# Kernel tuning notes

Measured on AMD Instinct MI355X. Metric: run time of the kernel, lower is better.

The kernel has to match this reference:

```python
import jax, jax.numpy as jnp
import numpy as np

B, T, C, H = 4, 2048, 1024, 16
HS = C // H  # head size 64
LN_EPS = 1e-5


def setup_inputs() -> dict:
    key = jax.random.key(0)
    ks = jax.random.split(key, 14)
    s = lambda fan_in: 1.0 / np.sqrt(fan_in)
    return {
        "x": jax.random.normal(ks[0], (B, T, C), jnp.float32),
        # weights stored [in, out] (transposed vs torch nn.Linear) for y = x @ W + b
        "c_attn_w": jax.random.normal(ks[1], (C, 3 * C), jnp.float32) * s(C),
        "c_attn_b": jnp.zeros((3 * C,), jnp.float32),
        "c_proj_w": jax.random.normal(ks[2], (C, C), jnp.float32) * s(C),
        "c_proj_b": jnp.zeros((C,), jnp.float32),
        "fc_w": jax.random.normal(ks[3], (C, 4 * C), jnp.float32) * s(C),
        "fc_b": jnp.zeros((4 * C,), jnp.float32),
        "proj_w": jax.random.normal(ks[4], (4 * C, C), jnp.float32) * s(4 * C),
        "proj_b": jnp.zeros((C,), jnp.float32),
        "ln1_g": jnp.ones((C,), jnp.float32),
        "ln1_b": jnp.zeros((C,), jnp.float32),
        "ln2_g": jnp.ones((C,), jnp.float32),
        "ln2_b": jnp.zeros((C,), jnp.float32),
    }


def layer_norm(x, g, b):
    mu = jnp.mean(x, axis=-1, keepdims=True)
    var = jnp.var(x, axis=-1, keepdims=True)
    return (x - mu) * jax.lax.rsqrt(var + LN_EPS) * g + b


def attention(x, c_attn_w, c_attn_b, c_proj_w, c_proj_b):
    Bs, Ts, Cs = x.shape
    qkv = x @ c_attn_w + c_attn_b  # (B,T,3C)
    q, k, v = jnp.split(qkv, 3, axis=-1)
    q = q.reshape(Bs, Ts, H, HS).transpose(0, 2, 1, 3)  # (B,H,T,hs)
    k = k.reshape(Bs, Ts, H, HS).transpose(0, 2, 1, 3)
    v = v.reshape(Bs, Ts, H, HS).transpose(0, 2, 1, 3)
    wei = jnp.einsum("bhqd,bhkd->bhqk", q, k) * (1.0 / np.sqrt(HS))
    causal = jnp.tril(jnp.ones((Ts, Ts), bool))
    wei = jnp.where(causal, wei, -jnp.inf)
    wei = jax.nn.softmax(wei, axis=-1)
    out = jnp.einsum("bhqk,bhkd->bhqd", wei, v)
    out = out.transpose(0, 2, 1, 3).reshape(Bs, Ts, Cs)
    return out @ c_proj_w + c_proj_b


def mlp(x, fc_w, fc_b, proj_w, proj_b):
    h = jax.nn.gelu(x @ fc_w + fc_b, approximate=True)
    return h @ proj_w + proj_b


def reference(x, c_attn_w, c_attn_b, c_proj_w, c_proj_b, fc_w, fc_b, proj_w, proj_b, ln1_g, ln1_b, ln2_g, ln2_b):
    x = x + attention(layer_norm(x, ln1_g, ln1_b), c_attn_w, c_attn_b, c_proj_w, c_proj_b)
    out = x + mlp(layer_norm(x, ln2_g, ln2_b), fc_w, fc_b, proj_w, proj_b)
    return out
```

## Files before the change

### kernel.cpp

```cpp
#include <hip/hip_runtime.h>

typedef unsigned short u16;
typedef __attribute__((ext_vector_type(8))) short bf16x8;
typedef __attribute__((ext_vector_type(4))) float f32x4;

#define SC_LOG2E 0.18033688011112043f
#define MB_LOG2E 17.31234049066756f

__device__ __forceinline__ float b2f(u16 u) {
  union { unsigned int i; float f; } v; v.i = ((unsigned int)u) << 16; return v.f;
}
__device__ __forceinline__ u16 f2b(float f) {
  unsigned int x = __float_as_uint(f);
  unsigned int r = (x + 0x7fffu + ((x >> 16) & 1u)) >> 16;
  return (u16)r;
}

#define GLOAD_LDS16(g, l)                                                              \
  __builtin_amdgcn_global_load_lds((const __attribute__((address_space(1))) void*)(g), \
                                   (__attribute__((address_space(3))) void*)(l), 16, 0, 0)

__global__ __launch_bounds__(256) void transpose_cast_kernel(const float* __restrict__ in,
                                                             u16* __restrict__ out,
                                                             int K, int N) {
  __shared__ float tile[64][65];
  const int tid = threadIdx.x;
  const int n0 = blockIdx.x * 64, k0 = blockIdx.y * 64;
#pragma unroll
  for (int it = 0; it < 4; ++it) {
    int lin = it * 256 + tid;
    int r = lin >> 4, c4 = (lin & 15) * 4;
    float4 v = *(const float4*)&in[(size_t)(k0 + r) * N + n0 + c4];
    tile[r][c4 + 0] = v.x; tile[r][c4 + 1] = v.y;
    tile[r][c4 + 2] = v.z; tile[r][c4 + 3] = v.w;
  }
  __syncthreads();
#pragma unroll
  for (int it = 0; it < 2; ++it) {
    int lin = it * 256 + tid;
    int r = lin >> 3, c8 = (lin & 7) * 8;
    u16 tmp[8];
#pragma unroll
    for (int j = 0; j < 8; ++j) tmp[j] = f2b(tile[c8 + j][r]);
    *(uint4*)&out[(size_t)(n0 + r) * K + k0 + c8] = *(const uint4*)tmp;
  }
}

__global__ __launch_bounds__(256) void transpose_v_kernel(const u16* __restrict__ qkv,
                                                          u16* __restrict__ vt) {
  __shared__ float tl[64][65];
  const int tid = threadIdx.x;
  const int bh = blockIdx.y, b = bh >> 4, h = bh & 15;
  const int t0 = blockIdx.x * 64;
  const int voff = 2048 + h * 64;
#pragma unroll
  for (int it = 0; it < 2; ++it) {
    int lin = it * 256 + tid;
    int tt = lin >> 3, d8 = (lin & 7) * 8;
    uint4 v = *(const uint4*)&qkv[((size_t)b * 2048 + t0 + tt) * 3072 + voff + d8];
    const u16* p = (const u16*)&v;
#pragma unroll
    for (int j = 0; j < 8; ++j) tl[tt][d8 + j] = b2f(p[j]);
  }
  __syncthreads();
#pragma unroll
  for (int it = 0; it < 2; ++it) {
    int lin = it * 256 + tid;
    int d = lin >> 3, t8 = (lin & 7) * 8;
    u16 tmp[8];
#pragma unroll
    for (int j = 0; j < 8; ++j) tmp[j] = f2b(tl[t8 + j][d]);
    *(uint4*)&vt[((size_t)bh * 64 + d) * 2048 + t0 + t8] = *(const uint4*)tmp;
  }
}

template <bool INF32>
__global__ __launch_bounds__(256) void ln_kernel(const void* __restrict__ xv,
                                                 const float* __restrict__ g,
                                                 const float* __restrict__ b,
                                                 u16* __restrict__ o, int C) {
  const int row = blockIdx.x, tid = threadIdx.x;
  const int wave = tid >> 6, lane = tid & 63;
  const int base = tid * 4;
  float f[4];
  if (INF32) {
    float4 v = *(const float4*)((const float*)xv + (size_t)row * C + base);
    f[0] = v.x; f[1] = v.y; f[2] = v.z; f[3] = v.w;
  } else {
    ushort4 v = *(const ushort4*)((const u16*)xv + (size_t)row * C + base);
    f[0] = b2f(v.x); f[1] = b2f(v.y); f[2] = b2f(v.z); f[3] = b2f(v.w);
  }
  float s = f[0] + f[1] + f[2] + f[3];
  float q = f[0] * f[0] + f[1] * f[1] + f[2] * f[2] + f[3] * f[3];
#pragma unroll
  for (int off = 1; off < 64; off <<= 1) {
    s += __shfl_xor(s, off);
    q += __shfl_xor(q, off);
  }
  __shared__ float reds[4], redq[4];
  if (lane == 0) { reds[wave] = s; redq[wave] = q; }
  __syncthreads();
  float S = reds[0] + reds[1] + reds[2] + reds[3];
  float Q = redq[0] + redq[1] + redq[2] + redq[3];
  const float inv = 1.0f / (float)C;
  float mean = S * inv;
  float var = Q * inv - mean * mean;
  float rs = rsqrtf(var + 1e-5f);
  float4 gv = *(const float4*)&g[base];
  float4 bv = *(const float4*)&b[base];
  ushort4 ov;
  ov.x = f2b((f[0] - mean) * rs * gv.x + bv.x);
  ov.y = f2b((f[1] - mean) * rs * gv.y + bv.y);
  ov.z = f2b((f[2] - mean) * rs * gv.z + bv.z);
  ov.w = f2b((f[3] - mean) * rs * gv.w + bv.w);
  *(ushort4*)&o[(size_t)row * C + base] = ov;
}

__device__ __forceinline__ float gelu_fn(float v) {
  float a = 0.7978845608028654f * __builtin_fmaf(0.044715f * v * v, v, v);
  float t = __builtin_amdgcn_exp2f(a * -2.8853900817779268f);
  return v * __builtin_amdgcn_rcpf(1.0f + t);
}

template <bool GELU, int RESMODE, bool OUTF32>
__global__ __launch_bounds__(256) void gemm_kernel(const u16* __restrict__ A,
                                                   const u16* __restrict__ Bt,
                                                   const float* __restrict__ bias,
                                                   const void* __restrict__ res,
                                                   void* __restrict__ Cv,
                                                   int M, int N, int K) {
  __shared__ u16 As[128 * 64];
  __shared__ u16 Bs[128 * 64];
  const int tid = threadIdx.x;
  const int wave = tid >> 6, lane = tid & 63;
  const int lhi = lane >> 4, llo = lane & 15;
  const int sw = llo & 7;
  const int m0 = blockIdx.x * 128, n0 = blockIdx.y * 128;
  const int wr = (wave >> 1) * 64, wc = (wave & 1) * 64;

  f32x4 acc[4][4] = {};

  for (int k0 = 0; k0 < K; k0 += 64) {
#pragma unroll
    for (int p = 0; p < 4; ++p) {
      int s = p * 256 + tid;
      int r = s >> 3;
      int c = ((s & 7) ^ (r & 7)) * 8;
      GLOAD_LDS16(A + (size_t)(m0 + r) * K + k0 + c, As + s * 8);
      GLOAD_LDS16(Bt + (size_t)(n0 + r) * K + k0 + c, Bs + s * 8);
    }
    __syncthreads();
#pragma unroll
    for (int kk = 0; kk < 2; ++kk) {
      const int cp = ((kk * 4 + lhi) ^ sw) * 8;
      bf16x8 af[4], bf[4];
#pragma unroll
      for (int i = 0; i < 4; ++i)
        af[i] = *(const bf16x8*)&As[(wr + i * 16 + llo) * 64 + cp];
#pragma unroll
      for (int j = 0; j < 4; ++j)
        bf[j] = *(const bf16x8*)&Bs[(wc + j * 16 + llo) * 64 + cp];
#pragma unroll
      for (int i = 0; i < 4; ++i)
#pragma unroll
        for (int j = 0; j < 4; ++j)
          acc[i][j] = __builtin_amdgcn_mfma_f32_16x16x32_bf16(af[i], bf[j], acc[i][j], 0, 0, 0);
    }
    __syncthreads();
  }

#pragma unroll
  for (int i = 0; i < 4; ++i) {
    int row = m0 + wr + i * 16 + lhi * 4;
#pragma unroll
    for (int j = 0; j < 4; ++j) {
      int col = n0 + wc + j * 16 + llo;
      float bv = bias[col];
#pragma unroll
      for (int r = 0; r < 4; ++r) {
        float v = acc[i][j][r] + bv;
        if (GELU) v = gelu_fn(v);
        size_t idx = (size_t)(row + r) * N + col;
        if (RESMODE == 1) v += b2f(((const u16*)res)[idx]);
        if (RESMODE == 2) v += ((const float*)res)[idx];
        if (OUTF32) ((float*)Cv)[idx] = v;
        else ((u16*)Cv)[idx] = f2b(v);
      }
    }
  }
}

__global__ __launch_bounds__(512, 4) void attn_kernel(const u16* __restrict__ qkv,
                                                      const u16* __restrict__ vt,
                                                      u16* __restrict__ out) {
  __shared__ u16 Ks[64 * 68];
  __shared__ u16 Vs[64 * 68];
  __shared__ u16 Ps[128 * 68];
  const int tid = threadIdx.x;
  const int wave = tid >> 6, lane = tid & 63;
  const int lhi = lane >> 4, llo = lane & 15;
  const int pr = blockIdx.x;
  const int bh = blockIdx.y;
  const int b = bh >> 4, h = bh & 15;
  const size_t rowbase = (size_t)b * 2048;
  const int qoff = h * 64, koff = 1024 + h * 64;
  const u16* vtb = vt + (size_t)bh * 64 * 2048;
  const int sr = tid >> 3;
  const int sc = (tid & 7) * 8;

#pragma unroll
  for (int ph = 0; ph < 2; ++ph) {
    const int qtile = ph ? pr : (15 - pr);
    const int q0 = qtile * 128;
    const int qrow = q0 + wave * 16;

    bf16x8 qf[2];
#pragma unroll
    for (int kk = 0; kk < 2; ++kk) {
      uint4 v = *(const uint4*)&qkv[(rowbase + qrow + llo) * 3072 + qoff + kk * 32 + lhi * 8];
      qf[kk] = *(const bf16x8*)&v;
    }

    f32x4 oacc[4] = {};
    float l_st[4] = {};
    const int nkt = 2 * qtile + 2;

    uint4 pk = *(const uint4*)&qkv[(rowbase + sr) * 3072 + koff + sc];
    uint4 pv = *(const uint4*)&vtb[(size_t)sr * 2048 + sc];

    for (int kt = 0; kt < nkt; ++kt) {
      const int kt0 = kt * 64;
      __syncthreads();
      *(uint4*)&Ks[sr * 68 + sc] = pk;
      *(uint4*)&Vs[sr * 68 + sc] = pv;
      __syncthreads();
      if (kt + 1 < nkt) {
        const int nt0 = kt0 + 64;
        pk = *(const uint4*)&qkv[(rowbase + nt0 + sr) * 3072 + koff + sc];
        pv = *(const uint4*)&vtb[(size_t)sr * 2048 + nt0 + sc];
      }

      if (kt0 > qrow + 15) continue;

      f32x4 s[4] = {};
#pragma unroll
      for (int kk = 0; kk < 2; ++kk)
#pragma unroll
        for (int j = 0; j < 4; ++j) {
          bf16x8 kf = *(const bf16x8*)&Ks[(j * 16 + llo) * 68 + kk * 32 + lhi * 8];
          s[j] = __builtin_amdgcn_mfma_f32_16x16x32_bf16(qf[kk], kf, s[j], 0, 0, 0);
        }

      const bool msk = (kt0 + 63 > qrow);
      u16* psrow = &Ps[(wave * 16) * 68];
#pragma unroll
      for (int j = 0; j < 4; ++j) {
        const int key = kt0 + j * 16 + llo;
#pragma unroll
        for (int r = 0; r < 4; ++r) {
          float sv = s[j][r];
          if (msk) sv = (key <= qrow + lhi * 4 + r) ? sv : -1e30f;
          float p = __builtin_amdgcn_exp2f(__builtin_fmaf(sv, SC_LOG2E, -MB_LOG2E));
          l_st[r] += p;
          psrow[(lhi * 4 + r) * 68 + j * 16 + llo] = (u16)(__float_as_uint(p) >> 16);
        }
      }

#pragma unroll
      for (int kc = 0; kc < 2; ++kc) {
        bf16x8 pf = *(const bf16x8*)&Ps[(wave * 16 + llo) * 68 + kc * 32 + lhi * 8];
#pragma unroll
        for (int j4 = 0; j4 < 4; ++j4) {
          bf16x8 vf = *(const bf16x8*)&Vs[(j4 * 16 + llo) * 68 + kc * 32 + lhi * 8];
          oacc[j4] = __builtin_amdgcn_mfma_f32_16x16x32_bf16(pf, vf, oacc[j4], 0, 0, 0);
        }
      }
    }

#pragma unroll
    for (int r = 0; r < 4; ++r) {
      float v = l_st[r];
      v += __shfl_xor(v, 1);
      v += __shfl_xor(v, 2);
      v += __shfl_xor(v, 4);
      v += __shfl_xor(v, 8);
      l_st[r] = 1.0f / v;
    }
#pragma unroll
    for (int j4 = 0; j4 < 4; ++j4)
#pragma unroll
      for (int r = 0; r < 4; ++r) {
        size_t row = rowbase + qrow + lhi * 4 + r;
        out[row * 1024 + h * 64 + j4 * 16 + llo] = f2b(oacc[j4][r] * l_st[r]);
      }
  }
}

extern "C" void kernel_launch(void* const* d_in, const int* in_sizes, int n_in,
                              void* d_out, int out_size, void* d_ws, size_t ws_size,
                              hipStream_t stream) {
  const float* x        = (const float*)d_in[0];
  const float* c_attn_w = (const float*)d_in[1];
  const float* c_attn_b = (const float*)d_in[2];
  const float* c_proj_w = (const float*)d_in[3];
  const float* c_proj_b = (const float*)d_in[4];
  const float* fc_w     = (const float*)d_in[5];
  const float* fc_b     = (const float*)d_in[6];
  const float* proj_w   = (const float*)d_in[7];
  const float* proj_b   = (const float*)d_in[8];
  const float* ln1_g    = (const float*)d_in[9];
  const float* ln1_b    = (const float*)d_in[10];
  const float* ln2_g    = (const float*)d_in[11];
  const float* ln2_b    = (const float*)d_in[12];
  float* out = (float*)d_out;
  u16* ws = (u16*)d_ws;

  const size_t M = 8192;
  u16* ln_buf = ws;
  u16* qkv    = ln_buf + M * 1024;
  u16* x1     = qkv + M * 3072;
  u16* hbuf   = x1 + M * 1024;
  u16* wT_a   = hbuf + M * 4096;
  u16* wT_p   = wT_a + 3072 * 1024;
  u16* wT_f   = wT_p + 1024 * 1024;
  u16* wT_m   = wT_f + 4096 * 1024;
  u16* vt     = hbuf;

  dim3 blk(256);
  transpose_cast_kernel<<<dim3(48, 16), blk, 0, stream>>>(c_attn_w, wT_a, 1024, 3072);
  transpose_cast_kernel<<<dim3(16, 16), blk, 0, stream>>>(c_proj_w, wT_p, 1024, 1024);
  transpose_cast_kernel<<<dim3(64, 16), blk, 0, stream>>>(fc_w, wT_f, 1024, 4096);
  transpose_cast_kernel<<<dim3(16, 64), blk, 0, stream>>>(proj_w, wT_m, 4096, 1024);

  ln_kernel<true><<<8192, blk, 0, stream>>>(x, ln1_g, ln1_b, ln_buf, 1024);
  gemm_kernel<false, 0, false><<<dim3(64, 24), blk, 0, stream>>>(ln_buf, wT_a, c_attn_b, nullptr, qkv, 8192, 3072, 1024);
  transpose_v_kernel<<<dim3(32, 64), blk, 0, stream>>>(qkv, vt);
  attn_kernel<<<dim3(8, 64), dim3(512), 0, stream>>>(qkv, vt, ln_buf);
  gemm_kernel<false, 2, false><<<dim3(64, 8), blk, 0, stream>>>(ln_buf, wT_p, c_proj_b, x, x1, 8192, 1024, 1024);
  ln_kernel<false><<<8192, blk, 0, stream>>>(x1, ln2_g, ln2_b, ln_buf, 1024);
  gemm_kernel<true, 0, false><<<dim3(64, 32), blk, 0, stream>>>(ln_buf, wT_f, fc_b, nullptr, hbuf, 8192, 4096, 1024);
  gemm_kernel<false, 1, true><<<dim3(64, 8), blk, 0, stream>>>(hbuf, wT_m, proj_b, x1, out, 8192, 1024, 4096);
}
```

Before: 478.4 us.

## Add 256x256-tile double-buffered GEMM for QKV and FC projections

Adds a new GEMM kernel with 256x256 output tiles, 8 waves per block, and double-buffered LDS staging through direct global-to-LDS loads with an XOR swizzle. It is used for the two wide GEMMs (QKV and the FC layer with GELU). The larger tiles raise arithmetic intensity and cut redundant global loads, and loads for the next tiles overlap with MFMA work. The cost is 128KB of LDS and 128 accumulator registers per thread, which limits occupancy. Grid sizes also shrink to 384 and 512 blocks, which risks poor balance across CUs.

```diff
diff --git a/kernel.cpp b/kernel.cpp
--- a/kernel.cpp
+++ b/kernel.cpp
@@ -185,6 +185,91 @@
         if (RESMODE == 2) v += ((const float*)res)[idx];
         if (OUTF32) ((float*)Cv)[idx] = v;
         else ((u16*)Cv)[idx] = f2b(v);
+      }
+    }
+  }
+}
+
+template <bool GELU>
+__global__ __launch_bounds__(512, 2) void gemm256_kernel(const u16* __restrict__ A,
+                                                         const u16* __restrict__ Bt,
+                                                         const float* __restrict__ bias,
+                                                         u16* __restrict__ Cv,
+                                                         int M, int N, int K) {
+  __shared__ u16 As[2][256 * 64];
+  __shared__ u16 Bs[2][256 * 64];
+  const int tid = threadIdx.x;
+  const int wave = tid >> 6, lane = tid & 63;
+  const int lhi = lane >> 4, llo = lane & 15;
+  const int sw = llo & 7;
+  const int m0 = blockIdx.x * 256, n0 = blockIdx.y * 256;
+  const int wr = (wave >> 2) * 128, wc = (wave & 3) * 64;
+
+  f32x4 acc[8][4] = {};
+  const int nkt = K >> 6;
+
+  auto stage = [&](int b, int kt) {
+    const int k0 = kt * 64;
+#pragma unroll
+    for (int p = 0; p < 4; ++p) {
+      int s = p * 512 + tid;
+      int r = s >> 3;
+      int c = ((s & 7) ^ (r & 7)) * 8;
+      GLOAD_LDS16(A + (size_t)(m0 + r) * K + k0 + c, &As[b][s * 8]);
+      GLOAD_LDS16(Bt + (size_t)(n0 + r) * K + k0 + c, &Bs[b][s * 8]);
+    }
+  };
+
+  stage(0, 0);
+  stage(1, 1);
+  asm volatile("s_waitcnt vmcnt(8)" ::: "memory");
+  __builtin_amdgcn_s_barrier();
+
+  int cur = 0;
+  for (int kt = 0; kt < nkt; ++kt) {
+#pragma unroll
+    for (int kk = 0; kk < 2; ++kk) {
+      const int cp = ((kk * 4 + lhi) ^ sw) * 8;
+      bf16x8 af[8], bf[4];
+#pragma unroll
+      for (int i = 0; i < 8; ++i)
+        af[i] = *(const bf16x8*)&As[cur][(wr + i * 16 + llo) * 64 + cp];
+#pragma unroll
+      for (int j = 0; j < 4; ++j)
+        bf[j] = *(const bf16x8*)&Bs[cur][(wc + j * 16 + llo) * 64 + cp];
+      __builtin_amdgcn_s_setprio(1);
+#pragma unroll
+      for (int i = 0; i < 8; ++i)
+#pragma unroll
+        for (int j = 0; j < 4; ++j)
+          acc[i][j] = __builtin_amdgcn_mfma_f32_16x16x32_bf16(af[i], bf[j], acc[i][j], 0, 0, 0);
+      __builtin_amdgcn_s_setprio(0);
+    }
+    asm volatile("s_waitcnt lgkmcnt(0)" ::: "memory");
+    __builtin_amdgcn_s_barrier();
+    if (kt + 2 < nkt) {
+      stage(cur, kt + 2);
+      asm volatile("s_waitcnt vmcnt(8)" ::: "memory");
+      __builtin_amdgcn_s_barrier();
+    } else if (kt + 1 < nkt) {
+      asm volatile("s_waitcnt vmcnt(0)" ::: "memory");
+      __builtin_amdgcn_s_barrier();
+    }
+    cur ^= 1;
+  }
+
+#pragma unroll
+  for (int i = 0; i < 8; ++i) {
+    int row = m0 + wr + i * 16 + lhi * 4;
+#pragma unroll
+    for (int j = 0; j < 4; ++j) {
+      int col = n0 + wc + j * 16 + llo;
+      float bv = bias[col];
+#pragma unroll
+      for (int r = 0; r < 4; ++r) {
+        float v = acc[i][j][r] + bv;
+        if (GELU) v = gelu_fn(v);
+        Cv[(size_t)(row + r) * N + col] = f2b(v);
       }
     }
   }
@@ -333,11 +418,11 @@
   transpose_cast_kernel<<<dim3(16, 64), blk, 0, stream>>>(proj_w, wT_m, 4096, 1024);
 
   ln_kernel<true><<<8192, blk, 0, stream>>>(x, ln1_g, ln1_b, ln_buf, 1024);
-  gemm_kernel<false, 0, false><<<dim3(64, 24), blk, 0, stream>>>(ln_buf, wT_a, c_attn_b, nullptr, qkv, 8192, 3072, 1024);
+  gemm256_kernel<false><<<dim3(32, 12), dim3(512), 0, stream>>>(ln_buf, wT_a, c_attn_b, qkv, 8192, 3072, 1024);
   transpose_v_kernel<<<dim3(32, 64), blk, 0, stream>>>(qkv, vt);
   attn_kernel<<<dim3(8, 64), dim3(512), 0, stream>>>(qkv, vt, ln_buf);
   gemm_kernel<false, 2, false><<<dim3(64, 8), blk, 0, stream>>>(ln_buf, wT_p, c_proj_b, x, x1, 8192, 1024, 1024);
   ln_kernel<false><<<8192, blk, 0, stream>>>(x1, ln2_g, ln2_b, ln_buf, 1024);
-  gemm_kernel<true, 0, false><<<dim3(64, 32), blk, 0, stream>>>(ln_buf, wT_f, fc_b, nullptr, hbuf, 8192, 4096, 1024);
+  gemm256_kernel<true><<<dim3(32, 16), dim3(512), 0, stream>>>(ln_buf, wT_f, fc_b, hbuf, 8192, 4096, 1024);
   gemm_kernel<false, 1, true><<<dim3(64, 8), blk, 0, stream>>>(hbuf, wT_m, proj_b, x1, out, 8192, 1024, 4096);
 }
```

After: 482.1 us. Within noise of the previous version (+0.8%).
